# Optimization experiments

Measured on AMD Instinct MI355X. Metric: run time of the kernel, lower is better.

The kernel has to match this reference:

```python
import jax, jax.numpy as jnp
import numpy as np

N, E = 50000, 800000
IN_C, OUT_C, HEADS = 128, 16, 8
EDGE_DIM = 1
NEG_SLOPE = 0.2
LN_EPS = 1e-5


def setup_inputs() -> dict:
    key = jax.random.key(0)
    ks = jax.random.split(key, 12)
    s = 1.0 / np.sqrt(IN_C)
    HC = OUT_C * HEADS
    return {
        "x": jax.random.normal(ks[0], (N, IN_C), jnp.float32),
        "edge_index": jax.random.randint(ks[1], (2, E), 0, N, jnp.int32),
        "edge_attr": jax.random.normal(ks[2], (E, EDGE_DIM), jnp.float32),
        "W": jax.random.normal(ks[3], (IN_C, HC), jnp.float32) * s,
        "b": jnp.zeros((HC,), jnp.float32),
        "att_src": jax.random.normal(ks[4], (HEADS, OUT_C), jnp.float32) * s,
        "att_dst": jax.random.normal(ks[5], (HEADS, OUT_C), jnp.float32) * s,
        "att_edge": jax.random.normal(ks[6], (HEADS, OUT_C), jnp.float32) * s,
        "lin_edge_w": jax.random.normal(ks[7], (EDGE_DIM, HC), jnp.float32) * s,
        "lin_edge_b": jnp.zeros((HC,), jnp.float32),
        "gamma": jnp.ones((HC,), jnp.float32),
        "beta": jnp.zeros((HC,), jnp.float32),
    }


def _segment_softmax(logits, seg, num_segments):
    # numerically-stable softmax over edges grouped by destination node
    m = jax.ops.segment_max(logits, seg, num_segments=num_segments)
    ex = jnp.exp(logits - m[seg])
    z = jax.ops.segment_sum(ex, seg, num_segments=num_segments)
    return ex / (z[seg] + 1e-16)


def reference(x, edge_index, edge_attr, W, b, att_src, att_dst, att_edge,
              lin_edge_w, lin_edge_b, gamma, beta):
    n = x.shape[0]
    src, dst = edge_index[0], edge_index[1]
    # GAT conv: per-head transform, edge-indexed attention, segment softmax, scatter-add
    h = (x @ W).reshape(n, HEADS, OUT_C)                      # [N,H,C]
    a_src = jnp.einsum('nhc,hc->nh', h, att_src)              # [N,H]
    a_dst = jnp.einsum('nhc,hc->nh', h, att_dst)
    e = (edge_attr @ lin_edge_w + lin_edge_b).reshape(-1, HEADS, OUT_C)
    a_edge = jnp.einsum('ehc,hc->eh', e, att_edge)            # [E,H]
    logits = jax.nn.leaky_relu(a_src[src] + a_dst[dst] + a_edge, NEG_SLOPE)
    alpha = _segment_softmax(logits, dst, n)                  # [E,H]
    msg = alpha[..., None] * h[src]                           # [E,H,C]
    out = jax.ops.segment_sum(msg, dst, num_segments=n).reshape(n, -1) + b
    # residual (in_channels == heads*out_channels -> identity projection)
    out = out + x
    # LayerNorm + ELU (dropout is eval-mode identity)
    mu = jnp.mean(out, axis=-1, keepdims=True)
    var = jnp.var(out, axis=-1, keepdims=True)
    out = (out - mu) * jax.lax.rsqrt(var + LN_EPS) * gamma + beta
    return jax.nn.elu(out)
```

## Files before the change

kernel.cpp:

```cpp
#include <hip/hip_runtime.h>
#include <hip/hip_bf16.h>

#define N_NODES 50000
#define N_EDGES 800000
#define IN_C 128
#define HC 128
#define HEADS 8
#define NEG_SLOPE 0.2f
#define LN_EPS 1e-5f

#define LDH 136
#define ELL_CAP 64
#define GEMM_BLOCKS 782
#define FILL_BLOCKS 782
#define FUSED_BLOCKS (GEMM_BLOCKS + FILL_BLOCKS)

typedef __hip_bfloat16 bf16;
typedef __attribute__((ext_vector_type(8))) short short8;
typedef __attribute__((ext_vector_type(4))) float f32x4;

__device__ __forceinline__ float b2f(bf16 v) { return __bfloat162float(v); }

__device__ __forceinline__ unsigned short f2bf(float f) {
    unsigned u = __float_as_uint(f);
    return (unsigned short)((u + 0x7fffu + ((u >> 16) & 1u)) >> 16);
}
__device__ __forceinline__ float bf2f(unsigned s) {
    return __uint_as_float(s << 16);
}
__device__ __forceinline__ short8 pack8(float4 u, float4 v) {
    short8 r;
    r[0] = (short)f2bf(u.x); r[1] = (short)f2bf(u.y);
    r[2] = (short)f2bf(u.z); r[3] = (short)f2bf(u.w);
    r[4] = (short)f2bf(v.x); r[5] = (short)f2bf(v.y);
    r[6] = (short)f2bf(v.z); r[7] = (short)f2bf(v.w);
    return r;
}

__global__ __launch_bounds__(256) void prep(
    const float* __restrict__ W, unsigned short* __restrict__ Wt,
    int* __restrict__ cnt)
{
    int id = blockIdx.x * 256 + threadIdx.x;
    int k = id >> 7, n = id & 127;
    Wt[n * 128 + k] = f2bf(W[id]);
#pragma unroll
    for (int i = 0; i < 4; ++i) {
        int j = id + i * 16384;
        if (j < N_NODES) cnt[j] = 0;
    }
}

__global__ __launch_bounds__(256) void fused(
    const float* __restrict__ x, const unsigned short* __restrict__ Wt,
    const float* __restrict__ att_src, const float* __restrict__ att_dst,
    const int* __restrict__ ei, const float* __restrict__ edge_attr,
    int* __restrict__ cnt, unsigned int* __restrict__ ellp,
    unsigned short* __restrict__ h_out,
    float* __restrict__ a_src, float* __restrict__ a_dst)
{
    __shared__ short sH[4][16 * LDH];
    const int bid = blockIdx.x;
    const int t   = threadIdx.x;

    if (bid & 1) {
        const int fid = bid >> 1;
        const int e0  = (fid * 256 + t) * 4;
        if (e0 >= N_EDGES) return;
        const int4   s4 = *reinterpret_cast<const int4*>(ei + e0);
        const int4   d4 = *reinterpret_cast<const int4*>(ei + N_EDGES + e0);
        const float4 a4 = *reinterpret_cast<const float4*>(edge_attr + e0);

        int p0 = atomicAdd(&cnt[d4.x], 1);
        int p1 = atomicAdd(&cnt[d4.y], 1);
        int p2 = atomicAdd(&cnt[d4.z], 1);
        int p3 = atomicAdd(&cnt[d4.w], 1);
#define PUT(P, D, S, A)                                                    \
        if ((P) < ELL_CAP)                                                 \
            __builtin_nontemporal_store(                                   \
                (((unsigned)(S)) << 16) | (unsigned)f2bf(A),               \
                &ellp[((D) << 6) + (P)]);
        PUT(p0, d4.x, s4.x, a4.x)
        PUT(p1, d4.y, s4.y, a4.y)
        PUT(p2, d4.z, s4.z, a4.z)
        PUT(p3, d4.w, s4.w, a4.w)
#undef PUT
        return;
    }

    const int gid = bid >> 1;
    const int wv  = t >> 6;
    const int l   = t & 63;
    const int gw  = gid * 4 + wv;
    if (gw >= N_NODES / 16) return;

    const int n0   = gw * 16;
    const int mrow = l & 15;
    const int quad = l >> 4;

    short8 afrag[4];
    const float* xr = x + (size_t)(n0 + mrow) * IN_C + quad * 8;
#pragma unroll
    for (int ko = 0; ko < 4; ++ko) {
        float4 u = *reinterpret_cast<const float4*>(xr + ko * 32);
        float4 v = *reinterpret_cast<const float4*>(xr + ko * 32 + 4);
        afrag[ko] = pack8(u, v);
    }

    f32x4 acc[8];
#pragma unroll
    for (int nt = 0; nt < 8; ++nt) acc[nt] = (f32x4)0.f;
#pragma unroll
    for (int nt = 0; nt < 8; ++nt) {
        const unsigned short* wr = Wt + (nt * 16 + mrow) * 128 + quad * 8;
#pragma unroll
        for (int ko = 0; ko < 4; ++ko) {
            short8 bfr = *reinterpret_cast<const short8*>(wr + ko * 32);
            acc[nt] = __builtin_amdgcn_mfma_f32_16x16x32_bf16(afrag[ko], bfr, acc[nt], 0, 0, 0);
        }
    }

#pragma unroll
    for (int nt = 0; nt < 8; ++nt)
#pragma unroll
        for (int r = 0; r < 4; ++r)
            sH[wv][(quad * 4 + r) * LDH + nt * 16 + mrow] = (short)f2bf(acc[nt][r]);

#pragma unroll
    for (int i = 0; i < 4; ++i) {
        int row = i * 4 + (l >> 4);
        int col = (l & 15) * 8;
        short8 hv = *reinterpret_cast<const short8*>(&sH[wv][row * LDH + col]);
        *reinterpret_cast<short8*>(h_out + (size_t)(n0 + row) * HC + col) = hv;
    }

#pragma unroll
    for (int pp = 0; pp < 2; ++pp) {
        int p  = l + pp * 64;
        int m  = p >> 3;
        int hd = p & 7;
        float ssum = 0.f, dsum = 0.f;
#pragma unroll
        for (int c = 0; c < 16; ++c) {
            float hv = bf2f((unsigned short)sH[wv][m * LDH + hd * 16 + c]);
            ssum = fmaf(hv, att_src[hd * 16 + c], ssum);
            dsum = fmaf(hv, att_dst[hd * 16 + c], dsum);
        }
        a_src[(n0 + m) * HEADS + hd] = ssum;
        a_dst[(n0 + m) * HEADS + hd] = dsum;
    }
}


#define LROW(CE, HV, J, OFF, B0)                                           \
    { int cj_ = __builtin_amdgcn_ds_swizzle((int)(CE), OFF);               \
      size_t r_ = ((B0) + (J) < cn) ? (size_t)(((unsigned)cj_) >> 16) : 0; \
      (HV)[J] = h2[r_ * 64 + l]; }
#define LOADROWS(CE, HV, B0)                                               \
    LROW(CE, HV, 0,  24, B0) LROW(CE, HV, 1,  56, B0)                      \
    LROW(CE, HV, 2,  88, B0) LROW(CE, HV, 3, 120, B0)                      \
    LROW(CE, HV, 4, 152, B0) LROW(CE, HV, 5, 184, B0)                      \
    LROW(CE, HV, 6, 216, B0) LROW(CE, HV, 7, 248, B0)

#define FROW(EV, HV, J, OFF)                                               \
    { float evj_ = __uint_as_float((unsigned)__builtin_amdgcn_ds_swizzle(  \
          __float_as_int(EV), OFF));                                       \
      acc0 = fmaf(evj_, b2f((HV)[J].x), acc0);                             \
      acc1 = fmaf(evj_, b2f((HV)[J].y), acc1); }
#define FMAROWS(EV, HV)                                                    \
    FROW(EV, HV, 0,  24) FROW(EV, HV, 1,  56) FROW(EV, HV, 2,  88)        \
    FROW(EV, HV, 3, 120) FROW(EV, HV, 4, 152) FROW(EV, HV, 5, 184)        \
    FROW(EV, HV, 6, 216) FROW(EV, HV, 7, 248)

__global__ __launch_bounds__(256) void gather_node(
    const int* __restrict__ cnt, const unsigned int* __restrict__ ellp,
    const float* __restrict__ a_src, const float* __restrict__ a_dst,
    const bf16* __restrict__ h,
    const float* __restrict__ x, const float* __restrict__ bvec,
    const float* __restrict__ gamma, const float* __restrict__ beta,
    const float* __restrict__ att_edge, const float* __restrict__ lin_w,
    const float* __restrict__ lin_b,
    float* __restrict__ out)
{
    const int wave = threadIdx.x >> 6;
    const int l    = threadIdx.x & 63;
    const int n    = blockIdx.x * 4 + wave;
    const int hh   = l >> 3;
    const int jj   = l & 7;

    float ae0 = att_edge[2 * l], ae1 = att_edge[2 * l + 1];
    float p = ae0 * lin_w[2 * l] + ae1 * lin_w[2 * l + 1];
    float q = ae0 * lin_b[2 * l] + ae1 * lin_b[2 * l + 1];
#pragma unroll
    for (int off = 1; off <= 4; off <<= 1) {
        p += __shfl_xor(p, off, 64);
        q += __shfl_xor(q, off, 64);
    }
    const float2 bv = *reinterpret_cast<const float2*>(bvec + 2 * l);
    const float2 gv = *reinterpret_cast<const float2*>(gamma + 2 * l);
    const float2 be = *reinterpret_cast<const float2*>(beta + 2 * l);

    const float adq = a_dst[n * HEADS + hh] + q;
    const int   beg = n << 6;
    const int   cn  = min(cnt[n], ELL_CAP);

    float zp = 0.f, acc0 = 0.f, acc1 = 0.f;
    const __hip_bfloat162* h2 = reinterpret_cast<const __hip_bfloat162*>(h);

    if (cn > 0) {
        unsigned ce_c = ellp[beg + jj];
        float    as_c = a_src[(ce_c >> 16) * HEADS + hh];
        __hip_bfloat162 hv_c[8], hv_n[8];
        LOADROWS(ce_c, hv_c, 0)

        for (int bs = 0; ; bs += 8) {
            const unsigned ce   = ce_c;
            const float    as   = as_c;
            const bool     last = (bs + 8 >= cn);
            if (!last) {
                ce_c = ellp[beg + bs + 8 + jj];
                LOADROWS(ce_c, hv_n, bs + 8)
                as_c = a_src[(ce_c >> 16) * HEADS + hh];
            }
            const float ea = bf2f(ce & 0xffffu);
            float lg = fmaf(ea, p, as + adq);
            lg = fmaxf(lg, NEG_SLOPE * lg);
            const float ev = (bs + jj < cn) ? __expf(lg) : 0.f;
            zp += ev;
            FMAROWS(ev, hv_c)
            if (last) break;
#pragma unroll
            for (int j = 0; j < 8; ++j) hv_c[j] = hv_n[j];
        }
    }

    float z = zp;
    z += __shfl_xor(z, 1, 64);
    z += __shfl_xor(z, 2, 64);
    z += __shfl_xor(z, 4, 64);
    const float rz = 1.f / (z + 1e-16f);
    acc0 *= rz;
    acc1 *= rz;

    const size_t idx = (size_t)n * HC + 2 * l;
    const float2 xv = *reinterpret_cast<const float2*>(x + idx);
    float v0 = acc0 + xv.x + bv.x;
    float v1 = acc1 + xv.y + bv.y;
    float s1 = v0 + v1, s2 = v0 * v0 + v1 * v1;
#pragma unroll
    for (int off = 32; off >= 1; off >>= 1) {
        s1 += __shfl_xor(s1, off, 64);
        s2 += __shfl_xor(s2, off, 64);
    }
    const float mean = s1 * (1.f / HC);
    const float var  = s2 * (1.f / HC) - mean * mean;
    const float inv  = rsqrtf(var + LN_EPS);
    float y0 = (v0 - mean) * inv * gv.x + be.x;
    float y1 = (v1 - mean) * inv * gv.y + be.y;
    y0 = y0 > 0.f ? y0 : expm1f(y0);
    y1 = y1 > 0.f ? y1 : expm1f(y1);
    *reinterpret_cast<float2*>(out + idx) = make_float2(y0, y1);
}

extern "C" void kernel_launch(void* const* d_in, const int* in_sizes, int n_in,
                              void* d_out, int out_size, void* d_ws, size_t ws_size,
                              hipStream_t stream)
{
    const float* x         = (const float*)d_in[0];
    const int*   ei        = (const int*)d_in[1];
    const float* edge_attr = (const float*)d_in[2];
    const float* W         = (const float*)d_in[3];
    const float* b         = (const float*)d_in[4];
    const float* att_src   = (const float*)d_in[5];
    const float* att_dst   = (const float*)d_in[6];
    const float* att_edge  = (const float*)d_in[7];
    const float* lin_w     = (const float*)d_in[8];
    const float* lin_b     = (const float*)d_in[9];
    const float* gamma     = (const float*)d_in[10];
    const float* beta      = (const float*)d_in[11];

    char* ws = (char*)d_ws;
    bf16*  h     = (bf16*)ws;  ws += (size_t)N_NODES * HC * sizeof(bf16);
    float* a_src = (float*)ws; ws += (size_t)N_NODES * HEADS * sizeof(float);
    float* a_dst = (float*)ws; ws += (size_t)N_NODES * HEADS * sizeof(float);
    int*   cnt   = (int*)ws;   ws += (size_t)N_NODES * sizeof(int);
    unsigned short* Wt = (unsigned short*)ws;
    ws += (size_t)128 * 128 * sizeof(unsigned short);
    unsigned int* ellp = (unsigned int*)ws;
    ws += (size_t)(N_NODES * ELL_CAP + 64) * sizeof(unsigned int);

    prep<<<64, 256, 0, stream>>>(W, Wt, cnt);

    fused<<<FUSED_BLOCKS, 256, 0, stream>>>(
        x, Wt, att_src, att_dst, ei, edge_attr, cnt, ellp,
        (unsigned short*)h, a_src, a_dst);

    gather_node<<<N_NODES / 4, 256, 0, stream>>>(
        cnt, ellp, a_src, a_dst, h, x, b, gamma, beta,
        att_edge, lin_w, lin_b, (float*)d_out);
}
```

Measured before the change: 188.1 us.

## Partition ELL fill by destination modulo 8 with permuted counter layout

The ELL fill blocks are regrouped so that each group of 8 blocks rereads a chunk of 8192 edges, and each block handles only the edges whose destination mod 8 matches its sub-index. Counters are permuted so that each residue class sits in a contiguous region. The aim is to keep each block's atomics and ELL writes in a smaller, localized address range, likely to improve L2/XCD locality since blocks are dispatched round-robin across 8 XCDs. The cost is that edge-index and attribute loads are repeated 8 times, branches diverge, and the nontemporal store hint is dropped.

```diff
diff --git a/kernel.cpp b/kernel.cpp
--- a/kernel.cpp
+++ b/kernel.cpp
@@ -11,15 +11,17 @@
 
 #define LDH 136
 #define ELL_CAP 64
-#define GEMM_BLOCKS 782
-#define FILL_BLOCKS 782
-#define FUSED_BLOCKS (GEMM_BLOCKS + FILL_BLOCKS)
+#define CHUNK_E 8192
+#define N_CHUNKS 98
+#define FUSED_BLOCKS 1568
+#define CNT_SIZE 50048
 
 typedef __hip_bfloat16 bf16;
 typedef __attribute__((ext_vector_type(8))) short short8;
 typedef __attribute__((ext_vector_type(4))) float f32x4;
 
 __device__ __forceinline__ float b2f(bf16 v) { return __bfloat162float(v); }
+__device__ __forceinline__ int cperm(int n) { return (n & 7) * 6256 + (n >> 3); }
 
 __device__ __forceinline__ unsigned short f2bf(float f) {
     unsigned u = __float_as_uint(f);
@@ -47,7 +49,7 @@
 #pragma unroll
     for (int i = 0; i < 4; ++i) {
         int j = id + i * 16384;
-        if (j < N_NODES) cnt[j] = 0;
+        if (j < CNT_SIZE) cnt[j] = 0;
     }
 }
 
@@ -62,33 +64,37 @@
     __shared__ short sH[4][16 * LDH];
     const int bid = blockIdx.x;
     const int t   = threadIdx.x;
-
-    if (bid & 1) {
-        const int fid = bid >> 1;
-        const int e0  = (fid * 256 + t) * 4;
-        if (e0 >= N_EDGES) return;
-        const int4   s4 = *reinterpret_cast<const int4*>(ei + e0);
-        const int4   d4 = *reinterpret_cast<const int4*>(ei + N_EDGES + e0);
-        const float4 a4 = *reinterpret_cast<const float4*>(edge_attr + e0);
-
-        int p0 = atomicAdd(&cnt[d4.x], 1);
-        int p1 = atomicAdd(&cnt[d4.y], 1);
-        int p2 = atomicAdd(&cnt[d4.z], 1);
-        int p3 = atomicAdd(&cnt[d4.w], 1);
-#define PUT(P, D, S, A)                                                    \
-        if ((P) < ELL_CAP)                                                 \
-            __builtin_nontemporal_store(                                   \
-                (((unsigned)(S)) << 16) | (unsigned)f2bf(A),               \
-                &ellp[((D) << 6) + (P)]);
-        PUT(p0, d4.x, s4.x, a4.x)
-        PUT(p1, d4.y, s4.y, a4.y)
-        PUT(p2, d4.z, s4.z, a4.z)
-        PUT(p3, d4.w, s4.w, a4.w)
-#undef PUT
+    const int grp = bid >> 3;
+    const int sub = bid & 7;
+
+    if (grp & 1) {
+        const int chunk = grp >> 1;
+        const int base  = chunk * CHUNK_E;
+#define PROC(D, S, A)                                                      \
+        if ((((D) & 7) == sub)) {                                          \
+            int p_ = atomicAdd(&cnt[cperm(D)], 1);                         \
+            if (p_ < ELL_CAP)                                              \
+                ellp[((D) << 6) + p_] =                                    \
+                    (((unsigned)(S)) << 16) | (unsigned)f2bf(A);           \
+        }
+#pragma unroll
+        for (int i = 0; i < 8; ++i) {
+            const int e = base + i * 1024 + t * 4;
+            if (e < N_EDGES) {
+                const int4   s4 = *reinterpret_cast<const int4*>(ei + e);
+                const int4   d4 = *reinterpret_cast<const int4*>(ei + N_EDGES + e);
+                const float4 a4 = *reinterpret_cast<const float4*>(edge_attr + e);
+                PROC(d4.x, s4.x, a4.x)
+                PROC(d4.y, s4.y, a4.y)
+                PROC(d4.z, s4.z, a4.z)
+                PROC(d4.w, s4.w, a4.w)
+            }
+        }
+#undef PROC
         return;
     }
 
-    const int gid = bid >> 1;
+    const int gid = (grp >> 1) * 8 + sub;
     const int wv  = t >> 6;
     const int l   = t & 63;
     const int gw  = gid * 4 + wv;
@@ -202,7 +208,7 @@
 
     const float adq = a_dst[n * HEADS + hh] + q;
     const int   beg = n << 6;
-    const int   cn  = min(cnt[n], ELL_CAP);
+    const int   cn  = min(cnt[cperm(n)], ELL_CAP);
 
     float zp = 0.f, acc0 = 0.f, acc1 = 0.f;
     const __hip_bfloat162* h2 = reinterpret_cast<const __hip_bfloat162*>(h);
@@ -283,7 +289,7 @@
     bf16*  h     = (bf16*)ws;  ws += (size_t)N_NODES * HC * sizeof(bf16);
     float* a_src = (float*)ws; ws += (size_t)N_NODES * HEADS * sizeof(float);
     float* a_dst = (float*)ws; ws += (size_t)N_NODES * HEADS * sizeof(float);
-    int*   cnt   = (int*)ws;   ws += (size_t)N_NODES * sizeof(int);
+    int*   cnt   = (int*)ws;   ws += (size_t)CNT_SIZE * sizeof(int);
     unsigned short* Wt = (unsigned short*)ws;
     ws += (size_t)128 * 128 * sizeof(unsigned short);
     unsigned int* ellp = (unsigned int*)ws;
```

Result: no change. 187.7 us (-0.2%).

## Replace global atomic ELL fill with two-pass bucketed binning through shared memory

Applied to the files above, without the earlier changes.

The ELL adjacency build changes from per-edge global atomics on per-node counters to two passes. First, each fill block bins its 1024 edges into 64 destination-range buckets using shared-memory atomics and writes packed 64-bit records into a staging area held in the output buffer. A new ebuild kernel then scans each bucket per sub-range and fills the ELL using shared-memory counters, which removes scattered global atomics and the counter-zeroing in prep. In exchange it adds an extra kernel launch and extra staging traffic, and any edges past the per-segment cap of 48 are dropped.

```diff
diff --git a/kernel.cpp b/kernel.cpp
--- a/kernel.cpp
+++ b/kernel.cpp
@@ -11,13 +11,17 @@
 
 #define LDH 136
 #define ELL_CAP 64
-#define GEMM_BLOCKS 782
-#define FILL_BLOCKS 782
-#define FUSED_BLOCKS (GEMM_BLOCKS + FILL_BLOCKS)
+#define NBUCK 64
+#define BRANGE 784
+#define BINBLK 784
+#define SEGCAP 48
+#define FUSED_BLOCKS 1568
+#define SUBR 8
 
 typedef __hip_bfloat16 bf16;
 typedef __attribute__((ext_vector_type(8))) short short8;
 typedef __attribute__((ext_vector_type(4))) float f32x4;
+typedef unsigned long long u64;
 
 __device__ __forceinline__ float b2f(bf16 v) { return __bfloat162float(v); }
 
@@ -38,57 +42,60 @@
 }
 
 __global__ __launch_bounds__(256) void prep(
-    const float* __restrict__ W, unsigned short* __restrict__ Wt,
-    int* __restrict__ cnt)
+    const float* __restrict__ W, unsigned short* __restrict__ Wt)
 {
     int id = blockIdx.x * 256 + threadIdx.x;
     int k = id >> 7, n = id & 127;
     Wt[n * 128 + k] = f2bf(W[id]);
-#pragma unroll
-    for (int i = 0; i < 4; ++i) {
-        int j = id + i * 16384;
-        if (j < N_NODES) cnt[j] = 0;
-    }
 }
 
 __global__ __launch_bounds__(256) void fused(
     const float* __restrict__ x, const unsigned short* __restrict__ Wt,
     const float* __restrict__ att_src, const float* __restrict__ att_dst,
     const int* __restrict__ ei, const float* __restrict__ edge_attr,
-    int* __restrict__ cnt, unsigned int* __restrict__ ellp,
+    u64* __restrict__ binned, int* __restrict__ bcnt,
     unsigned short* __restrict__ h_out,
     float* __restrict__ a_src, float* __restrict__ a_dst)
 {
     __shared__ short sH[4][16 * LDH];
+    __shared__ int   lcnt[NBUCK];
     const int bid = blockIdx.x;
     const int t   = threadIdx.x;
-
-    if (bid & 1) {
-        const int fid = bid >> 1;
-        const int e0  = (fid * 256 + t) * 4;
-        if (e0 >= N_EDGES) return;
-        const int4   s4 = *reinterpret_cast<const int4*>(ei + e0);
-        const int4   d4 = *reinterpret_cast<const int4*>(ei + N_EDGES + e0);
-        const float4 a4 = *reinterpret_cast<const float4*>(edge_attr + e0);
-
-        int p0 = atomicAdd(&cnt[d4.x], 1);
-        int p1 = atomicAdd(&cnt[d4.y], 1);
-        int p2 = atomicAdd(&cnt[d4.z], 1);
-        int p3 = atomicAdd(&cnt[d4.w], 1);
-#define PUT(P, D, S, A)                                                    \
-        if ((P) < ELL_CAP)                                                 \
-            __builtin_nontemporal_store(                                   \
-                (((unsigned)(S)) << 16) | (unsigned)f2bf(A),               \
-                &ellp[((D) << 6) + (P)]);
-        PUT(p0, d4.x, s4.x, a4.x)
-        PUT(p1, d4.y, s4.y, a4.y)
-        PUT(p2, d4.z, s4.z, a4.z)
-        PUT(p3, d4.w, s4.w, a4.w)
-#undef PUT
+    const int grp = bid >> 3;
+    const int sub = bid & 7;
+
+    if (grp & 1) {
+        const int blk = (grp >> 1) * 8 + sub;
+        if (t < NBUCK) lcnt[t] = 0;
+        __syncthreads();
+
+        const int e0 = blk * 1024 + t * 4;
+        if (e0 < N_EDGES) {
+            const int4   s4 = *reinterpret_cast<const int4*>(ei + e0);
+            const int4   d4 = *reinterpret_cast<const int4*>(ei + N_EDGES + e0);
+            const float4 a4 = *reinterpret_cast<const float4*>(edge_attr + e0);
+#define BIN1(D, S, A)                                                      \
+            {                                                              \
+                int b_ = (D) / BRANGE;                                     \
+                int p_ = atomicAdd(&lcnt[b_], 1);                          \
+                if (p_ < SEGCAP)                                           \
+                    binned[(size_t)((b_ * BINBLK + blk) * SEGCAP + p_)] =  \
+                        ((u64)(unsigned)((D) - b_ * BRANGE) << 32) |       \
+                        ((u64)(unsigned)(S) << 16) | (u64)f2bf(A);         \
+            }
+            BIN1(d4.x, s4.x, a4.x)
+            BIN1(d4.y, s4.y, a4.y)
+            BIN1(d4.z, s4.z, a4.z)
+            BIN1(d4.w, s4.w, a4.w)
+#undef BIN1
+        }
+        __syncthreads();
+        if (t < NBUCK && blk < 782)
+            bcnt[t * BINBLK + blk] = min(lcnt[t], SEGCAP);
         return;
     }
 
-    const int gid = bid >> 1;
+    const int gid = (grp >> 1) * 8 + sub;
     const int wv  = t >> 6;
     const int l   = t & 63;
     const int gw  = gid * 4 + wv;
@@ -148,6 +155,46 @@
         }
         a_src[(n0 + m) * HEADS + hd] = ssum;
         a_dst[(n0 + m) * HEADS + hd] = dsum;
+    }
+}
+
+__global__ __launch_bounds__(256) void ebuild(
+    const u64* __restrict__ binned, const int* __restrict__ bcnt,
+    unsigned int* __restrict__ ellp, int* __restrict__ cnt)
+{
+    __shared__ unsigned short sb[BINBLK];
+    __shared__ int lc[98];
+    const int t = threadIdx.x;
+    const int b = blockIdx.x >> 3;
+    const int s = blockIdx.x & 7;
+    const int nbase = b * BRANGE + s * 98;
+
+    for (int i = t; i < 782; i += 256) sb[i] = (unsigned short)bcnt[b * BINBLK + i];
+    for (int i = t; i < 98; i += 256) lc[i] = 0;
+    __syncthreads();
+
+    const u64* seg = binned + (size_t)b * (BINBLK * SEGCAP);
+    for (int q = t; q < 782 * SEGCAP; q += 256) {
+        const int blk = q / SEGCAP;
+        const int sl  = q - blk * SEGCAP;
+        if (sl < (int)sb[blk]) {
+            const u64 e = seg[q];
+            const int dl = (int)(e >> 32);
+            const unsigned ul = (unsigned)(dl - s * 98);
+            if (ul < 98u) {
+                const int n = b * BRANGE + dl;
+                if (n < N_NODES) {
+                    int p = atomicAdd(&lc[ul], 1);
+                    if (p < ELL_CAP)
+                        ellp[((size_t)n << 6) + p] = (unsigned)e;
+                }
+            }
+        }
+    }
+    __syncthreads();
+    if (t < 98) {
+        const int n = nbase + t;
+        if (n < N_NODES) cnt[n] = min(lc[t], ELL_CAP);
     }
 }
 
@@ -288,12 +335,17 @@
     ws += (size_t)128 * 128 * sizeof(unsigned short);
     unsigned int* ellp = (unsigned int*)ws;
     ws += (size_t)(N_NODES * ELL_CAP + 64) * sizeof(unsigned int);
-
-    prep<<<64, 256, 0, stream>>>(W, Wt, cnt);
+    int* bcnt = (int*)ws;
+    ws += (size_t)NBUCK * BINBLK * sizeof(int);
+    u64* binned = (u64*)d_out;
+
+    prep<<<64, 256, 0, stream>>>(W, Wt);
 
     fused<<<FUSED_BLOCKS, 256, 0, stream>>>(
-        x, Wt, att_src, att_dst, ei, edge_attr, cnt, ellp,
+        x, Wt, att_src, att_dst, ei, edge_attr, binned, bcnt,
         (unsigned short*)h, a_src, a_dst);
+
+    ebuild<<<NBUCK * SUBR, 256, 0, stream>>>(binned, bcnt, ellp, cnt);
 
     gather_node<<<N_NODES / 4, 256, 0, stream>>>(
         cnt, ellp, a_src, a_dst, h, x, b, gamma, beta,
```

Result: slower. 253.4 us (+34.7%).
